# Kernel optimization log

Measured on AMD Instinct MI355X. Metric: run time of the kernel, lower is better.

## Reference

```python
import jax, jax.numpy as jnp
import numpy as np

N, E, IN, H, L = 100000, 1600000, 128, 64, 3


def setup_inputs() -> dict:
    key = jax.random.key(0)
    ks = jax.random.split(key, 4)
    x = jax.random.normal(ks[0], (N, IN), dtype=jnp.float32)
    edge_index = jax.random.randint(ks[1], (2, E), 0, N, dtype=jnp.int32)
    enc_w = jax.random.normal(ks[2], (IN, H), dtype=jnp.float32) * 0.05
    enc_b = jnp.zeros((H,), jnp.float32)
    conv_w = jax.random.normal(ks[3], (L, H, H), dtype=jnp.float32) * 0.05
    conv_b = jnp.zeros((L, H), jnp.float32)
    return {"x": x, "edge_index": edge_index, "enc_w": enc_w, "enc_b": enc_b,
            "conv_w": conv_w, "conv_b": conv_b}


def _nuc(m):
    # nuclear norm of [N, C] via eigvals of the small C x C Gram matrix
    g = m.T @ m
    ev = jnp.linalg.eigvalsh(g)
    return jnp.sum(jnp.sqrt(jnp.clip(ev, 0.0, None)))


def _rank_diff(x):
    xn = x / _nuc(x)
    i = jnp.argmax(jnp.sum(jnp.abs(xn), axis=1))
    j = jnp.argmax(jnp.sum(jnp.abs(xn), axis=0))
    m0 = jnp.take(xn, i, axis=0)[None, :]   # [1, C]
    m1 = jnp.take(xn, j, axis=1)[:, None]   # [N, 1]
    m0 = jnp.where(jnp.take(m0[0], j) < 0.0, -m0, m0)
    xh = m1 @ m0
    xh = xh / _nuc(xh)
    return _nuc(xn - xh)


def _dirichlet(x, src, dst, deg, rw):
    # edges (src, dst) already include self loops; deg = degree(src)
    xn = x / jnp.linalg.norm(x)
    if rw:
        d = xn[src] - xn[dst]
        e = jnp.sum(d * d)
    else:
        xs = xn * jax.lax.rsqrt(deg)[:, None]
        d = xs[src] - xs[dst]
        coef = jax.lax.rsqrt(deg[src] * deg[dst])
        e = jnp.sum(coef * jnp.sum(d * d, axis=1))
    return 0.5 * e


def reference(x, edge_index, enc_w, enc_b, conv_w, conv_b):
    n = x.shape[0]
    loops = jnp.arange(n, dtype=edge_index.dtype)
    src = jnp.concatenate([edge_index[0], loops])
    dst = jnp.concatenate([edge_index[1], loops])
    ones = jnp.ones(src.shape[0], x.dtype)
    deg_dst = jax.ops.segment_sum(ones, dst, num_segments=n)   # GCN norm degree
    dis = jax.lax.rsqrt(deg_dst)
    norm = dis[src] * dis[dst]
    deg_src = jax.ops.segment_sum(ones, src, num_segments=n)   # dirichlet degree

    h = x @ enc_w + enc_b                                      # encoder
    energies = [_dirichlet(jax.lax.stop_gradient(h), src, dst, deg_src, rw=False)]
    energies_sym = []
    ranks = []
    for i in range(L):
        # GCNConv: linear -> gather -> sym-normalized scatter-add -> bias
        xw = h @ conv_w[i]
        msg = xw[src] * norm[:, None]
        h = jax.ops.segment_sum(msg, dst, num_segments=n) + conv_b[i]
        h = jax.nn.relu(h)
        hs = jax.lax.stop_gradient(h)
        energies.append(_dirichlet(hs, src, dst, deg_src, rw=True))
        energies_sym.append(_dirichlet(hs, src, dst, deg_src, rw=False))
        ranks.append(_rank_diff(hs))
    return h, jnp.stack(energies), jnp.stack(energies_sym), jnp.stack(ranks)
```

## Files before the change

kernel.cpp:

```cpp
#include <hip/hip_runtime.h>

#define WF 64

__device__ inline float wredsum(float v) {
#pragma unroll
  for (int m = 32; m; m >>= 1) v += __shfl_xor(v, m, WF);
  return v;
}
__device__ inline float4 wredsum4(float4 v) {
#pragma unroll
  for (int m = 32; m; m >>= 1) {
    v.x += __shfl_xor(v.x, m, WF);
    v.y += __shfl_xor(v.y, m, WF);
    v.z += __shfl_xor(v.z, m, WF);
    v.w += __shfl_xor(v.w, m, WF);
  }
  return v;
}
__device__ inline float wredmin(float v) {
#pragma unroll
  for (int m = 32; m; m >>= 1) v = fminf(v, __shfl_xor(v, m, WF));
  return v;
}
__device__ inline float wredmax(float v) {
#pragma unroll
  for (int m = 32; m; m >>= 1) v = fmaxf(v, __shfl_xor(v, m, WF));
  return v;
}

__device__ inline float fastrcp(float x) {
  float r;
  asm("v_rcp_f32 %0, %1" : "=v"(r) : "v"(x));
  return r;
}

__device__ inline void atomAddF(float* p, float v) { unsafeAtomicAdd(p, v); }

__global__ __launch_bounds__(256) void k_init(int* degs, int* degd, float* G,
                                              float* colsum, float* scal, int n) {
  int i = blockIdx.x * 256 + threadIdx.x;
  if (i < n) { degs[i] = 1; degd[i] = 1; }
  if (i < 3 * 4096) G[i] = 0.f;
  if (i < 3 * 64) colsum[i] = 0.f;
  if (i < 64) scal[i] = 0.f;
}

__global__ __launch_bounds__(256) void k_deg(const int* src, const int* dst,
                                             int* degs, int* degd, int e) {
  int i = blockIdx.x * 256 + threadIdx.x;
  int stride = gridDim.x * 256;
  for (; i < e; i += stride) {
    atomicAdd(&degs[src[i]], 1);
    atomicAdd(&degd[dst[i]], 1);
  }
}

__global__ __launch_bounds__(256) void k_nodescal(const int* degs, const int* degd,
                                                  float4* cn4, float* degsum, int n) {
  int i = blockIdx.x * 256 + threadIdx.x;
  if (i < n) {
    float fs = (float)degs[i], fd = (float)degd[i];
    float rs_ = rsqrtf(fs);
    float4 v;
    v.x = rsqrtf(fd);
    v.y = 1.f / fs;
    v.z = rs_;
    v.w = rs_ * rs_ * rs_;
    cn4[i] = v;
    degsum[i] = fs + fd;
  }
}

__global__ __launch_bounds__(256) void k_scan1(const int* degd, int* start, int* bsum, int n) {
  __shared__ int sb[256];
  int t = threadIdx.x, i = blockIdx.x * 256 + t;
  int v = (i < n) ? degd[i] : 0;
  sb[t] = v;
  __syncthreads();
  for (int off = 1; off < 256; off <<= 1) {
    int add = (t >= off) ? sb[t - off] : 0;
    __syncthreads();
    sb[t] += add;
    __syncthreads();
  }
  if (i < n) start[i] = sb[t] - v;
  if (t == 255) bsum[blockIdx.x] = sb[255];
}

__global__ __launch_bounds__(512) void k_scan2(int* bsum, int nb) {
  __shared__ int sb[512];
  int t = threadIdx.x;
  int v = (t < nb) ? bsum[t] : 0;
  sb[t] = v;
  __syncthreads();
  for (int off = 1; off < 512; off <<= 1) {
    int add = (t >= off) ? sb[t - off] : 0;
    __syncthreads();
    sb[t] += add;
    __syncthreads();
  }
  if (t < nb) bsum[t] = sb[t] - v;
}

__global__ __launch_bounds__(256) void k_scan3(int* start, const int* bsum, int* cursor,
                                               int n, int total) {
  int i = blockIdx.x * 256 + threadIdx.x;
  if (i < n) {
    int v = start[i] + bsum[i >> 8];
    start[i] = v;
    cursor[i] = v;
  }
  if (i == 0) start[n] = total;
}

__global__ __launch_bounds__(256) void k_scatter(const int* src, const int* dst, int* cursor,
                                                 int* csr, int e, int n) {
  int i = blockIdx.x * 256 + threadIdx.x;
  int tot = e + n;
  if (i >= tot) return;
  int s, d;
  if (i < e) { s = src[i]; d = dst[i]; } else { s = i - e; d = i - e; }
  int pos = atomicAdd(&cursor[d], 1);
  csr[pos] = s;
}

__global__ __launch_bounds__(256) void k_enc(const float* __restrict__ x,
                                             const float* __restrict__ W,
                                             const float* __restrict__ b,
                                             const float4* __restrict__ cn4,
                                             float* __restrict__ X,
                                             float* __restrict__ nsq,
                                             float4* __restrict__ P, int n) {
  __shared__ float Wl[128 * 64];
  for (int idx = threadIdx.x; idx < 128 * 64; idx += 256) Wl[idx] = W[idx];
  __syncthreads();
  int w = threadIdx.x >> 6, c = threadIdx.x & 63;
  float bc = b[c];
  for (int node = blockIdx.x * 4 + w; node < n; node += gridDim.x * 4) {
    const float4* xr4 = (const float4*)(x + (size_t)node * 128);
    float acc = bc;
#pragma unroll
    for (int k4 = 0; k4 < 32; k4++) {
      float4 xv = xr4[k4];
      acc += xv.x * Wl[(k4 * 4 + 0) * 64 + c];
      acc += xv.y * Wl[(k4 * 4 + 1) * 64 + c];
      acc += xv.z * Wl[(k4 * 4 + 2) * 64 + c];
      acc += xv.w * Wl[(k4 * 4 + 3) * 64 + c];
    }
    X[(size_t)node * 64 + c] = acc;
    float r = wredsum(acc * acc);
    if (c == 0) {
      nsq[node] = r;
      float4 c4 = cn4[node];
      P[node] = make_float4(c4.x, c4.y, c4.z, r * c4.w);
    }
  }
}

template <int AGGC>
__device__ inline void gather4(const float* __restrict__ H, const float4* __restrict__ P,
                               const int* __restrict__ csr, int k0, int k1, int g, int l16,
                               float4& agg0, float4& agg1, float4& aggC,
                               float& su, float& sv) {
  int kk = k0 + g;
  int last = k1 - 1;
  int s0 = csr[min(kk, last)];
  int s1 = csr[min(kk + 4, last)];
  int s2 = csr[min(kk + 8, last)];
  int s3 = csr[min(kk + 12, last)];
  while (kk < k1) {
    int kn = kk + 16;
    float4 h0 = *(const float4*)(H + (size_t)s0 * 64 + 4 * l16);
    float4 h1 = *(const float4*)(H + (size_t)s1 * 64 + 4 * l16);
    float4 h2 = *(const float4*)(H + (size_t)s2 * 64 + 4 * l16);
    float4 h3 = *(const float4*)(H + (size_t)s3 * 64 + 4 * l16);
    float4 Q0 = P[s0], Q1 = P[s1], Q2 = P[s2], Q3 = P[s3];
    s0 = csr[min(kn, last)];
    s1 = csr[min(kn + 4, last)];
    s2 = csr[min(kn + 8, last)];
    s3 = csr[min(kn + 12, last)];
    float m1 = (kk + 4 < k1) ? 1.f : 0.f;
    float m2 = (kk + 8 < k1) ? 1.f : 0.f;
    float m3 = (kk + 12 < k1) ? 1.f : 0.f;
    agg0.x += h0.x; agg0.y += h0.y; agg0.z += h0.z; agg0.w += h0.w;
    agg1.x = fmaf(h0.x, Q0.y, agg1.x); agg1.y = fmaf(h0.y, Q0.y, agg1.y);
    agg1.z = fmaf(h0.z, Q0.y, agg1.z); agg1.w = fmaf(h0.w, Q0.y, agg1.w);
    if (AGGC) {
      aggC.x = fmaf(h0.x, Q0.x, aggC.x); aggC.y = fmaf(h0.y, Q0.x, aggC.y);
      aggC.z = fmaf(h0.z, Q0.x, aggC.z); aggC.w = fmaf(h0.w, Q0.x, aggC.w);
    }
    su += Q0.w; sv += Q0.z;
    {
      float y = Q1.y * m1;
      agg0.x = fmaf(h1.x, m1, agg0.x); agg0.y = fmaf(h1.y, m1, agg0.y);
      agg0.z = fmaf(h1.z, m1, agg0.z); agg0.w = fmaf(h1.w, m1, agg0.w);
      agg1.x = fmaf(h1.x, y, agg1.x); agg1.y = fmaf(h1.y, y, agg1.y);
      agg1.z = fmaf(h1.z, y, agg1.z); agg1.w = fmaf(h1.w, y, agg1.w);
      if (AGGC) {
        float xq = Q1.x * m1;
        aggC.x = fmaf(h1.x, xq, aggC.x); aggC.y = fmaf(h1.y, xq, aggC.y);
        aggC.z = fmaf(h1.z, xq, aggC.z); aggC.w = fmaf(h1.w, xq, aggC.w);
      }
      su = fmaf(Q1.w, m1, su); sv = fmaf(Q1.z, m1, sv);
    }
    {
      float y = Q2.y * m2;
      agg0.x = fmaf(h2.x, m2, agg0.x); agg0.y = fmaf(h2.y, m2, agg0.y);
      agg0.z = fmaf(h2.z, m2, agg0.z); agg0.w = fmaf(h2.w, m2, agg0.w);
      agg1.x = fmaf(h2.x, y, agg1.x); agg1.y = fmaf(h2.y, y, agg1.y);
      agg1.z = fmaf(h2.z, y, agg1.z); agg1.w = fmaf(h2.w, y, agg1.w);
      if (AGGC) {
        float xq = Q2.x * m2;
        aggC.x = fmaf(h2.x, xq, aggC.x); aggC.y = fmaf(h2.y, xq, aggC.y);
        aggC.z = fmaf(h2.z, xq, aggC.z); aggC.w = fmaf(h2.w, xq, aggC.w);
      }
      su = fmaf(Q2.w, m2, su); sv = fmaf(Q2.z, m2, sv);
    }
    {
      float y = Q3.y * m3;
      agg0.x = fmaf(h3.x, m3, agg0.x); agg0.y = fmaf(h3.y, m3, agg0.y);
      agg0.z = fmaf(h3.z, m3, agg0.z); agg0.w = fmaf(h3.w, m3, agg0.w);
      agg1.x = fmaf(h3.x, y, agg1.x); agg1.y = fmaf(h3.y, y, agg1.y);
      agg1.z = fmaf(h3.z, y, agg1.z); agg1.w = fmaf(h3.w, y, agg1.w);
      if (AGGC) {
        float xq = Q3.x * m3;
        aggC.x = fmaf(h3.x, xq, aggC.x); aggC.y = fmaf(h3.y, xq, aggC.y);
        aggC.z = fmaf(h3.z, xq, aggC.z); aggC.w = fmaf(h3.w, xq, aggC.w);
      }
      su = fmaf(Q3.w, m3, su); sv = fmaf(Q3.z, m3, sv);
    }
    kk = kn;
  }
}

__global__ __launch_bounds__(256) void k_convpass(
    const float* __restrict__ H, const float4* __restrict__ P,
    const float* __restrict__ nsq, const float* __restrict__ degsum,
    const float4* __restrict__ cn4, const int* __restrict__ start,
    const int* __restrict__ csr, const float* __restrict__ W,
    const float* __restrict__ bias, float* __restrict__ T,
    float4* __restrict__ Pn, float* __restrict__ nsqN,
    float* __restrict__ scal5, float* __restrict__ G, float* __restrict__ colsum,
    float* __restrict__ bmv, int* __restrict__ bmi, int n) {
  __shared__ float Wl[4096];
  __shared__ float rowbuf[4][64];
  __shared__ float red[4][5];
  __shared__ float colred[4][64];
  __shared__ float mvs[4];
  __shared__ int mis[4];
  int t = threadIdx.x, w = t >> 6, lane = t & 63, g = lane >> 4, l16 = lane & 15;
  for (int i = t; i < 4096; i += 256) Wl[i] = W[i];
  __syncthreads();
  float a0 = 0.f, a1 = 0.f, a2 = 0.f, a3 = 0.f, a4 = 0.f;
  float Greg[16];
#pragma unroll
  for (int k = 0; k < 16; k++) Greg[k] = 0.f;
  float cacc = 0.f, best = -1.f;
  int bi = 0;
  float bc = bias[lane];
  int wid = blockIdx.x * 4 + w, nw = gridDim.x * 4;
  int iters = (n + nw - 1) / nw;
  for (int it = 0; it < iters; it++) {
    int d = wid + it * nw;
    bool valid = d < n;
    float tv = 0.f;
    if (valid) {
      int k0 = start[d], k1 = start[d + 1];
      float4 hd = *(const float4*)(H + (size_t)d * 64 + 4 * l16);
      float4 pd = P[d];
      float nqd = nsq[d];
      float dsum = degsum[d];
      float4 agg0 = {0.f, 0.f, 0.f, 0.f};
      float4 agg1 = {0.f, 0.f, 0.f, 0.f};
      float4 aggC = {0.f, 0.f, 0.f, 0.f};
      float su = 0.f, sv = 0.f;
      gather4<1>(H, P, csr, k0, k1, g, l16, agg0, agg1, aggC, su, sv);
      float td0 = agg0.x * hd.x + agg0.y * hd.y + agg0.z * hd.z + agg0.w * hd.w;
      float td1 = agg1.x * hd.x + agg1.y * hd.y + agg1.z * hd.z + agg1.w * hd.w;
      float4 r4 = wredsum4(make_float4(td0, td1, su, sv));
      float dot1 = r4.x, dot2 = r4.y;
      su = r4.z * 0.0625f;
      sv = r4.w * 0.0625f;
      a0 += dsum * nqd;
      a1 += dot1;
      a2 += pd.z * su + pd.w * sv;
      a3 += pd.y * dot2;
      a4 += nqd;
      aggC.x += __shfl_xor(aggC.x, 16); aggC.y += __shfl_xor(aggC.y, 16);
      aggC.z += __shfl_xor(aggC.z, 16); aggC.w += __shfl_xor(aggC.w, 16);
      aggC.x += __shfl_xor(aggC.x, 32); aggC.y += __shfl_xor(aggC.y, 32);
      aggC.z += __shfl_xor(aggC.z, 32); aggC.w += __shfl_xor(aggC.w, 32);
      float mv = 0.f;
#pragma unroll
      for (int kq = 0; kq < 16; kq++) {
        float ax = __shfl(aggC.x, kq, 16);
        float ay = __shfl(aggC.y, kq, 16);
        float az = __shfl(aggC.z, kq, 16);
        float aw = __shfl(aggC.w, kq, 16);
        mv += ax * Wl[(4 * kq + 0) * 64 + lane];
        mv += ay * Wl[(4 * kq + 1) * 64 + lane];
        mv += az * Wl[(4 * kq + 2) * 64 + lane];
        mv += aw * Wl[(4 * kq + 3) * 64 + lane];
      }
      tv = fmaxf(fmaf(pd.x, mv, bc), 0.f);
      T[(size_t)d * 64 + lane] = tv;
      float r = wredsum(tv * tv);
      float atv = fabsf(tv);
      cacc += atv;
      float rsum = wredsum(atv);
      if (rsum > best) { best = rsum; bi = d; }
      if (lane == 0) {
        nsqN[d] = r;
        float4 c4 = cn4[d];
        Pn[d] = make_float4(c4.x, c4.y, c4.z, r * c4.w);
      }
    }
    rowbuf[w][lane] = tv;
    __syncthreads();
#pragma unroll
    for (int rr = 0; rr < 4; rr++) {
      float hj = rowbuf[rr][lane];
#pragma unroll
      for (int k = 0; k < 16; k++) Greg[k] = fmaf(rowbuf[rr][w + 4 * k], hj, Greg[k]);
    }
    __syncthreads();
  }
#pragma unroll
  for (int k = 0; k < 16; k++) atomAddF(&G[(w + 4 * k) * 64 + lane], Greg[k]);
  colred[w][lane] = cacc;
  if (lane == 0) {
    red[w][0] = a0; red[w][1] = a1; red[w][2] = a2; red[w][3] = a3; red[w][4] = a4;
    mvs[w] = best; mis[w] = bi;
  }
  __syncthreads();
  if (t < 64) {
    float cs = colred[0][t] + colred[1][t] + colred[2][t] + colred[3][t];
    atomAddF(&colsum[t], cs);
  }
  if (t == 0) {
#pragma unroll
    for (int j = 0; j < 5; j++)
      atomAddF(&scal5[j], red[0][j] + red[1][j] + red[2][j] + red[3][j]);
    float bv = mvs[0]; int bix = mis[0];
    for (int q = 1; q < 4; q++)
      if (mvs[q] > bv || (mvs[q] == bv && mis[q] < bix)) { bv = mvs[q]; bix = mis[q]; }
    bmv[blockIdx.x] = bv;
    bmi[blockIdx.x] = bix;
  }
}

__global__ __launch_bounds__(64) void k_finalize(const float* T, const float* bmv,
                                                 const int* bmi, int nblocks,
                                                 const float* colsum, float* rowslot,
                                                 int* jstar, int n) {
  int t = threadIdx.x;
  float bv = -1.f;
  int bix = 0x7fffffff;
  for (int b = t; b < nblocks; b += 64) {
    float v = bmv[b]; int ix = bmi[b];
    if (v > bv || (v == bv && ix < bix)) { bv = v; bix = ix; }
  }
#pragma unroll
  for (int m = 32; m; m >>= 1) {
    float ov = __shfl_xor(bv, m); int oi = __shfl_xor(bix, m);
    if (ov > bv || (ov == bv && oi < bix)) { bv = ov; bix = oi; }
  }
  float cv = colsum[t];
  int cj = t;
#pragma unroll
  for (int m = 32; m; m >>= 1) {
    float ov = __shfl_xor(cv, m); int oj = __shfl_xor(cj, m);
    if (ov > cv || (ov == cv && oj < cj)) { cv = ov; cj = oj; }
  }
  if (t == 0) jstar[0] = cj;
  rowslot[t] = T[(size_t)bix * 64 + t];
}

__device__ float tridiag_sumsqrt(float (*A)[65], float* vbuf, float* wbuf,
                                 float (*wpart)[64], float2* de, float* esh, int t) {
  bool w0 = (t < 64);
  int lane = t & 63, w4 = t >> 6;
  for (int k = 0; k < 62; k++) {
    float beta = 0.f;
    if (w0) {
      float acol = A[t][k];
      float xs = (t >= k + 2) ? acol : 0.f;
      float sigma = wredsum(xs * xs);
      float x1 = __shfl(acol, k + 1, WF);
      float alpha = -copysignf(sqrtf(fmaf(x1, x1, sigma)), x1);
      float v1 = x1 - alpha;
      float vv = fmaf(v1, v1, sigma);
      beta = (vv > 1e-37f) ? 2.f / vv : 0.f;
      vbuf[t] = (t == k + 1) ? v1 : xs;
      if (t == 0) esh[k] = alpha;
    }
    __syncthreads();
    {
      float s0 = 0.f, s1 = 0.f, s2 = 0.f, s3 = 0.f;
#pragma unroll
      for (int i2 = 0; i2 < 4; i2++) {
        int j = w4 + 16 * i2;
        s0 = fmaf(A[lane][j], vbuf[j], s0);
        s1 = fmaf(A[lane][j + 4], vbuf[j + 4], s1);
        s2 = fmaf(A[lane][j + 8], vbuf[j + 8], s2);
        s3 = fmaf(A[lane][j + 12], vbuf[j + 12], s3);
      }
      wpart[w4][lane] = (s0 + s1) + (s2 + s3);
    }
    __syncthreads();
    if (w0) {
      float p = beta * (wpart[0][t] + wpart[1][t] + wpart[2][t] + wpart[3][t]);
      float dot = wredsum(vbuf[t] * p);
      float K = 0.5f * beta * dot;
      wbuf[t] = fmaf(-K, vbuf[t], p);
    }
    __syncthreads();
    {
      float vj = vbuf[lane], wj = wbuf[lane];
#pragma unroll
      for (int i2 = 0; i2 < 16; i2++) {
        int i = w4 + 4 * i2;
        A[i][lane] -= vbuf[i] * wj + wbuf[i] * vj;
      }
    }
    __syncthreads();
  }
  if (t == 0) { esh[62] = A[63][62]; esh[63] = 0.f; }
  __syncthreads();
  float gmin = 0.f, gmax = 0.f;
  if (w0) {
    float dt = A[t][t];
    float ep = (t >= 1) ? esh[t - 1] : 0.f;
    float en = (t <= 62) ? esh[t] : 0.f;
    de[t] = make_float2(dt, ep * ep);
    float rad = fabsf(ep) + fabsf(en);
    gmin = wredmin(dt - rad);
    gmax = wredmax(dt + rad);
  }
  __syncthreads();
  float lam = 0.f;
  if (w0) {
    float range = gmax - gmin;
    float lo = gmin - 1e-3f * range - 1e-30f;
    float hi = gmax + 1e-3f * range + 1e-30f;
    for (int it = 0; it < 30; it++) {
      float mid = 0.5f * (lo + hi);
      float q = de[0].x - mid;
      int cnt = (q < 0.f) ? 1 : 0;
      for (int i = 1; i < 64; i++) {
        float2 dc = de[i];
        float qq = (dc.x - mid) - dc.y * fastrcp(q);
        q = (fabsf(qq) < 1e-30f) ? -1e-30f : qq;
        cnt += (q < 0.f) ? 1 : 0;
      }
      if (cnt > t) hi = mid; else lo = mid;
    }
    lam = 0.5f * (lo + hi);
  }
  float svv = w0 ? sqrtf(fmaxf(lam, 0.f)) : 0.f;
  return wredsum(svv);
}

__global__ __launch_bounds__(256, 4) void k_final(
    const float* __restrict__ H, const float4* __restrict__ P,
    const float* __restrict__ nsq, const float* __restrict__ degsum,
    const int* __restrict__ start, const int* __restrict__ csr,
    float* __restrict__ scal5, const float* __restrict__ Gbase,
    const float* __restrict__ rowslot, const int* __restrict__ jstar,
    float* __restrict__ rankOut, int n, int nbE) {
  __shared__ float A[64][65];
  __shared__ float vbuf[64], wbuf[64], esh[64];
  __shared__ float wpart[4][64];
  __shared__ float2 de[64];
  __shared__ float u[64], m0[64];
  __shared__ float shn;
  __shared__ float red[4][5];
  int t = threadIdx.x, w = t >> 6, lane = t & 63, g = lane >> 4, l16 = lane & 15;
  if (blockIdx.x < 3) {
    int l = blockIdx.x;
    const float* Gl = Gbase + l * 4096;
    for (int idx = t; idx < 4096; idx += 256) A[idx >> 6][idx & 63] = Gl[idx];
    __syncthreads();
    float nuc1 = tridiag_sumsqrt(A, vbuf, wbuf, wpart, de, esh, t);
    if (t == 0) shn = nuc1;
    __syncthreads();
    float s = 1.f / shn;
    int js = jstar[l];
    if (t < 64) {
      float rv = rowslot[l * 64 + t];
      float rn2 = wredsum(rv * rv);
      float sign = (rowslot[l * 64 + js] < 0.f) ? -1.f : 1.f;
      m0[t] = sign * rv * rsqrtf(rn2);
      u[t] = s * Gl[t * 64 + js] * rsqrtf(Gl[js * 64 + js]);
    }
    __syncthreads();
    float s2 = s * s;
    for (int idx = t; idx < 4096; idx += 256) {
      int i = idx >> 6, j = idx & 63;
      A[i][j] = s2 * Gl[idx] - u[i] * m0[j] - m0[i] * u[j] + m0[i] * m0[j];
    }
    __syncthreads();
    float nuc2 = tridiag_sumsqrt(A, vbuf, wbuf, wpart, de, esh, t);
    if (t == 0) rankOut[l] = nuc2;
    return;
  }
  float a0 = 0.f, a1 = 0.f, a2 = 0.f, a3 = 0.f, a4 = 0.f;
  int wid = (blockIdx.x - 3) * 4 + w, nw = nbE * 4;
  for (int d = wid; d < n; d += nw) {
    int k0 = start[d], k1 = start[d + 1];
    float4 hd = *(const float4*)(H + (size_t)d * 64 + 4 * l16);
    float4 pd = P[d];
    float nqd = nsq[d];
    float dsum = degsum[d];
    float4 agg0 = {0.f, 0.f, 0.f, 0.f};
    float4 agg1 = {0.f, 0.f, 0.f, 0.f};
    float4 aggC = {0.f, 0.f, 0.f, 0.f};
    float su = 0.f, sv = 0.f;
    gather4<0>(H, P, csr, k0, k1, g, l16, agg0, agg1, aggC, su, sv);
    float td0 = agg0.x * hd.x + agg0.y * hd.y + agg0.z * hd.z + agg0.w * hd.w;
    float td1 = agg1.x * hd.x + agg1.y * hd.y + agg1.z * hd.z + agg1.w * hd.w;
    float4 r4 = wredsum4(make_float4(td0, td1, su, sv));
    a0 += dsum * nqd;
    a1 += r4.x;
    a2 += pd.z * (r4.z * 0.0625f) + pd.w * (r4.w * 0.0625f);
    a3 += pd.y * r4.y;
    a4 += nqd;
  }
  if (lane == 0) {
    red[w][0] = a0; red[w][1] = a1; red[w][2] = a2; red[w][3] = a3; red[w][4] = a4;
  }
  __syncthreads();
  if (t == 0) {
#pragma unroll
    for (int j = 0; j < 5; j++)
      atomAddF(&scal5[j], red[0][j] + red[1][j] + red[2][j] + red[3][j]);
  }
}

__global__ __launch_bounds__(64) void k_epi(const float* scal, float* outsc) {
  if (threadIdx.x == 0) {
    for (int st = 0; st < 4; st++) {
      const float* a = scal + 5 * st;
      float inv = 1.f / a[4];
      float rw = 0.5f * (a[0] - 2.f * a[1]) * inv;
      float sym = 0.5f * (a[2] - 2.f * a[3]) * inv;
      if (st == 0) outsc[0] = sym;
      else { outsc[st] = rw; outsc[3 + st] = sym; }
    }
    for (int l = 0; l < 3; l++) outsc[7 + l] = scal[20 + l];
  }
}

extern "C" void kernel_launch(void* const* d_in, const int* in_sizes, int n_in,
                              void* d_out, int out_size, void* d_ws, size_t ws_size,
                              hipStream_t stream) {
  const float* x      = (const float*)d_in[0];
  const int*   ei     = (const int*)d_in[1];
  const float* enc_w  = (const float*)d_in[2];
  const float* enc_b  = (const float*)d_in[3];
  const float* conv_w = (const float*)d_in[4];
  const float* conv_b = (const float*)d_in[5];
  const int n = in_sizes[0] / 128;
  const int e = in_sizes[1] / 2;
  const int* src = ei;
  const int* dst = ei + e;
  float* OUT = (float*)d_out;
  float* outsc = OUT + (size_t)n * 64;

  char* p = (char*)d_ws;
  auto alloc = [&](size_t bytes) -> char* {
    char* r = p;
    p += (bytes + 255) & ~size_t(255);
    return r;
  };
  float*  X      = (float*)alloc((size_t)n * 64 * 4);
  float*  Yf     = (float*)alloc((size_t)n * 64 * 4);
  int*    csr    = (int*)alloc((size_t)(e + n) * 4);
  int*    degs   = (int*)alloc((size_t)n * 4);
  int*    degd   = (int*)alloc((size_t)n * 4);
  float4* cn4    = (float4*)alloc((size_t)n * 16);
  float*  degsum = (float*)alloc((size_t)n * 4);
  int*    start  = (int*)alloc((size_t)(n + 1) * 4);
  int*    cursor = (int*)alloc((size_t)n * 4);
  int*    bsum   = (int*)alloc(4096);
  float*  nsqA   = (float*)alloc((size_t)n * 4);
  float*  nsqB   = (float*)alloc((size_t)n * 4);
  float4* Pa     = (float4*)alloc((size_t)n * 16);
  float4* Pb     = (float4*)alloc((size_t)n * 16);
  float*  G      = (float*)alloc(3 * 4096 * 4);
  float*  colsum = (float*)alloc(3 * 64 * 4);
  float*  bmv    = (float*)alloc(2048 * 4);
  int*    bmi    = (int*)alloc(2048 * 4);
  float*  rowslot= (float*)alloc(3 * 64 * 4);
  float*  scal   = (float*)alloc(64 * 4);
  int*    ij     = (int*)alloc(64 * 4);

  int nb = (n + 255) / 256;
  const int NBL = 2048;

  k_init<<<nb, 256, 0, stream>>>(degs, degd, G, colsum, scal, n);
  k_deg<<<2048, 256, 0, stream>>>(src, dst, degs, degd, e);
  k_nodescal<<<nb, 256, 0, stream>>>(degs, degd, cn4, degsum, n);
  k_scan1<<<nb, 256, 0, stream>>>(degd, start, bsum, n);
  k_scan2<<<1, 512, 0, stream>>>(bsum, nb);
  k_scan3<<<nb, 256, 0, stream>>>(start, bsum, cursor, n, e + n);
  k_scatter<<<(e + n + 255) / 256, 256, 0, stream>>>(src, dst, cursor, csr, e, n);
  k_enc<<<NBL, 256, 0, stream>>>(x, enc_w, enc_b, cn4, X, nsqA, Pa, n);

  k_convpass<<<NBL, 256, 0, stream>>>(X, Pa, nsqA, degsum, cn4, start, csr,
                                      conv_w, conv_b, Yf, Pb, nsqB,
                                      scal, G, colsum, bmv, bmi, n);
  k_finalize<<<1, 64, 0, stream>>>(Yf, bmv, bmi, NBL, colsum, rowslot, ij, n);

  k_convpass<<<NBL, 256, 0, stream>>>(Yf, Pb, nsqB, degsum, cn4, start, csr,
                                      conv_w + 4096, conv_b + 64, X, Pa, nsqA,
                                      scal + 5, G + 4096, colsum + 64, bmv, bmi, n);
  k_finalize<<<1, 64, 0, stream>>>(X, bmv, bmi, NBL, colsum + 64, rowslot + 64, ij + 1, n);

  k_convpass<<<NBL, 256, 0, stream>>>(X, Pa, nsqA, degsum, cn4, start, csr,
                                      conv_w + 2 * 4096, conv_b + 128, OUT, Pb, nsqB,
                                      scal + 10, G + 2 * 4096, colsum + 128, bmv, bmi, n);
  k_finalize<<<1, 64, 0, stream>>>(OUT, bmv, bmi, NBL, colsum + 128, rowslot + 128, ij + 2, n);

  k_final<<<NBL + 3, 256, 0, stream>>>(OUT, Pb, nsqB, degsum, start, csr,
                                       scal + 15, G, rowslot, ij, scal + 20, n, NBL);
  k_epi<<<1, 64, 0, stream>>>(scal, outsc);
}
```

Baseline: 1.435 ms.

## Overlap per-layer rank eigen-solve with next conv pass via extra block

Each layer's rank computation (two Householder tridiagonalizations and bisection eigenvalue solves) now runs in one extra block appended to the following conv pass, instead of three blocks serialized at the end in k_final. This hides the long single-block eigen-solve latency behind the bulk graph gather work. The Householder update also skips already-reduced rows and columns to cut redundant shared-memory work. Shared memory is unioned between the conv and rank layouts, and the grid-stride in convpass now uses nbC rather than gridDim.

```diff
diff --git a/kernel.cpp b/kernel.cpp
--- a/kernel.cpp
+++ b/kernel.cpp
@@ -35,6 +35,27 @@
 }
 
 __device__ inline void atomAddF(float* p, float v) { unsafeAtomicAdd(p, v); }
+
+struct ConvS {
+  float Wl[4096];
+  float rowbuf[4][64];
+  float red[4][5];
+  float colred[4][64];
+  float mvs[4];
+  int mis[4];
+};
+struct RankS {
+  float A[64][65];
+  float vbuf[64], wbuf[64], esh[64];
+  float wpart[4][64];
+  float2 de[64];
+  float u[64], m0[64];
+  float shn;
+};
+union SmemU {
+  ConvS c;
+  RankS r;
+};
 
 __global__ __launch_bounds__(256) void k_init(int* degs, int* degd, float* G,
                                               float* colsum, float* scal, int n) {
@@ -233,6 +254,119 @@
   }
 }
 
+__device__ float tridiag_sumsqrt(RankS& S, int t) {
+  bool w0 = (t < 64);
+  int lane = t & 63, w4 = t >> 6;
+  for (int k = 0; k < 62; k++) {
+    float beta = 0.f;
+    if (w0) {
+      float acol = S.A[t][k];
+      float xs = (t >= k + 2) ? acol : 0.f;
+      float sigma = wredsum(xs * xs);
+      float x1 = __shfl(acol, k + 1, WF);
+      float alpha = -copysignf(sqrtf(fmaf(x1, x1, sigma)), x1);
+      float v1 = x1 - alpha;
+      float vv = fmaf(v1, v1, sigma);
+      beta = (vv > 1e-37f) ? 2.f / vv : 0.f;
+      S.vbuf[t] = (t == k + 1) ? v1 : xs;
+      if (t == 0) S.esh[k] = alpha;
+    }
+    __syncthreads();
+    {
+      float s0 = 0.f, s1 = 0.f, s2 = 0.f, s3 = 0.f;
+#pragma unroll
+      for (int i2 = 0; i2 < 4; i2++) {
+        int j = w4 + 16 * i2;
+        if (j > k)      s0 = fmaf(S.A[lane][j], S.vbuf[j], s0);
+        if (j + 4 > k)  s1 = fmaf(S.A[lane][j + 4], S.vbuf[j + 4], s1);
+        if (j + 8 > k)  s2 = fmaf(S.A[lane][j + 8], S.vbuf[j + 8], s2);
+        if (j + 12 > k) s3 = fmaf(S.A[lane][j + 12], S.vbuf[j + 12], s3);
+      }
+      S.wpart[w4][lane] = (s0 + s1) + (s2 + s3);
+    }
+    __syncthreads();
+    if (w0) {
+      float p = beta * (S.wpart[0][t] + S.wpart[1][t] + S.wpart[2][t] + S.wpart[3][t]);
+      float dot = wredsum(S.vbuf[t] * p);
+      float K = 0.5f * beta * dot;
+      S.wbuf[t] = fmaf(-K, S.vbuf[t], p);
+    }
+    __syncthreads();
+    {
+      float vj = S.vbuf[lane], wj = S.wbuf[lane];
+#pragma unroll
+      for (int i2 = 0; i2 < 16; i2++) {
+        int i = w4 + 4 * i2;
+        if (i > k) S.A[i][lane] -= S.vbuf[i] * wj + S.wbuf[i] * vj;
+      }
+    }
+    __syncthreads();
+  }
+  if (t == 0) { S.esh[62] = S.A[63][62]; S.esh[63] = 0.f; }
+  __syncthreads();
+  float gmin = 0.f, gmax = 0.f;
+  if (w0) {
+    float dt = S.A[t][t];
+    float ep = (t >= 1) ? S.esh[t - 1] : 0.f;
+    float en = (t <= 62) ? S.esh[t] : 0.f;
+    S.de[t] = make_float2(dt, ep * ep);
+    float rad = fabsf(ep) + fabsf(en);
+    gmin = wredmin(dt - rad);
+    gmax = wredmax(dt + rad);
+  }
+  __syncthreads();
+  float lam = 0.f;
+  if (w0) {
+    float range = gmax - gmin;
+    float lo = gmin - 1e-3f * range - 1e-30f;
+    float hi = gmax + 1e-3f * range + 1e-30f;
+    for (int it = 0; it < 30; it++) {
+      float mid = 0.5f * (lo + hi);
+      float q = S.de[0].x - mid;
+      int cnt = (q < 0.f) ? 1 : 0;
+      for (int i = 1; i < 64; i++) {
+        float2 dc = S.de[i];
+        float qq = (dc.x - mid) - dc.y * fastrcp(q);
+        q = (fabsf(qq) < 1e-30f) ? -1e-30f : qq;
+        cnt += (q < 0.f) ? 1 : 0;
+      }
+      if (cnt > t) hi = mid; else lo = mid;
+    }
+    lam = 0.5f * (lo + hi);
+  }
+  float svv = w0 ? sqrtf(fmaxf(lam, 0.f)) : 0.f;
+  return wredsum(svv);
+}
+
+__device__ void rank_block(RankS& S, const float* __restrict__ Gl,
+                           const float* __restrict__ rowslot_l,
+                           const int* __restrict__ jstar_l,
+                           float* __restrict__ rankOut_l, int t) {
+  for (int idx = t; idx < 4096; idx += 256) S.A[idx >> 6][idx & 63] = Gl[idx];
+  __syncthreads();
+  float nuc1 = tridiag_sumsqrt(S, t);
+  if (t == 0) S.shn = nuc1;
+  __syncthreads();
+  float s = 1.f / S.shn;
+  int js = jstar_l[0];
+  if (t < 64) {
+    float rv = rowslot_l[t];
+    float rn2 = wredsum(rv * rv);
+    float sign = (rowslot_l[js] < 0.f) ? -1.f : 1.f;
+    S.m0[t] = sign * rv * rsqrtf(rn2);
+    S.u[t] = s * Gl[t * 64 + js] * rsqrtf(Gl[js * 64 + js]);
+  }
+  __syncthreads();
+  float s2 = s * s;
+  for (int idx = t; idx < 4096; idx += 256) {
+    int i = idx >> 6, j = idx & 63;
+    S.A[i][j] = s2 * Gl[idx] - S.u[i] * S.m0[j] - S.m0[i] * S.u[j] + S.m0[i] * S.m0[j];
+  }
+  __syncthreads();
+  float nuc2 = tridiag_sumsqrt(S, t);
+  if (t == 0) rankOut_l[0] = nuc2;
+}
+
 __global__ __launch_bounds__(256) void k_convpass(
     const float* __restrict__ H, const float4* __restrict__ P,
     const float* __restrict__ nsq, const float* __restrict__ degsum,
@@ -241,15 +375,16 @@
     const float* __restrict__ bias, float* __restrict__ T,
     float4* __restrict__ Pn, float* __restrict__ nsqN,
     float* __restrict__ scal5, float* __restrict__ G, float* __restrict__ colsum,
-    float* __restrict__ bmv, int* __restrict__ bmi, int n) {
-  __shared__ float Wl[4096];
-  __shared__ float rowbuf[4][64];
-  __shared__ float red[4][5];
-  __shared__ float colred[4][64];
-  __shared__ float mvs[4];
-  __shared__ int mis[4];
+    float* __restrict__ bmv, int* __restrict__ bmi, int n, int nbC,
+    const float* __restrict__ Gr, const float* __restrict__ rowslotR,
+    const int* __restrict__ jstarR, float* __restrict__ rankOutR) {
+  __shared__ SmemU sm;
   int t = threadIdx.x, w = t >> 6, lane = t & 63, g = lane >> 4, l16 = lane & 15;
-  for (int i = t; i < 4096; i += 256) Wl[i] = W[i];
+  if ((int)blockIdx.x >= nbC) {
+    rank_block(sm.r, Gr, rowslotR, jstarR, rankOutR, t);
+    return;
+  }
+  for (int i = t; i < 4096; i += 256) sm.c.Wl[i] = W[i];
   __syncthreads();
   float a0 = 0.f, a1 = 0.f, a2 = 0.f, a3 = 0.f, a4 = 0.f;
   float Greg[16];
@@ -258,7 +393,7 @@
   float cacc = 0.f, best = -1.f;
   int bi = 0;
   float bc = bias[lane];
-  int wid = blockIdx.x * 4 + w, nw = gridDim.x * 4;
+  int wid = blockIdx.x * 4 + w, nw = nbC * 4;
   int iters = (n + nw - 1) / nw;
   for (int it = 0; it < iters; it++) {
     int d = wid + it * nw;
@@ -297,10 +432,10 @@
         float ay = __shfl(aggC.y, kq, 16);
         float az = __shfl(aggC.z, kq, 16);
         float aw = __shfl(aggC.w, kq, 16);
-        mv += ax * Wl[(4 * kq + 0) * 64 + lane];
-        mv += ay * Wl[(4 * kq + 1) * 64 + lane];
-        mv += az * Wl[(4 * kq + 2) * 64 + lane];
-        mv += aw * Wl[(4 * kq + 3) * 64 + lane];
+        mv += ax * sm.c.Wl[(4 * kq + 0) * 64 + lane];
+        mv += ay * sm.c.Wl[(4 * kq + 1) * 64 + lane];
+        mv += az * sm.c.Wl[(4 * kq + 2) * 64 + lane];
+        mv += aw * sm.c.Wl[(4 * kq + 3) * 64 + lane];
       }
       tv = fmaxf(fmaf(pd.x, mv, bc), 0.f);
       T[(size_t)d * 64 + lane] = tv;
@@ -315,35 +450,38 @@
         Pn[d] = make_float4(c4.x, c4.y, c4.z, r * c4.w);
       }
     }
-    rowbuf[w][lane] = tv;
+    sm.c.rowbuf[w][lane] = tv;
     __syncthreads();
 #pragma unroll
     for (int rr = 0; rr < 4; rr++) {
-      float hj = rowbuf[rr][lane];
-#pragma unroll
-      for (int k = 0; k < 16; k++) Greg[k] = fmaf(rowbuf[rr][w + 4 * k], hj, Greg[k]);
+      float hj = sm.c.rowbuf[rr][lane];
+#pragma unroll
+      for (int k = 0; k < 16; k++) Greg[k] = fmaf(sm.c.rowbuf[rr][w + 4 * k], hj, Greg[k]);
     }
     __syncthreads();
   }
 #pragma unroll
   for (int k = 0; k < 16; k++) atomAddF(&G[(w + 4 * k) * 64 + lane], Greg[k]);
-  colred[w][lane] = cacc;
+  sm.c.colred[w][lane] = cacc;
   if (lane == 0) {
-    red[w][0] = a0; red[w][1] = a1; red[w][2] = a2; red[w][3] = a3; red[w][4] = a4;
-    mvs[w] = best; mis[w] = bi;
+    sm.c.red[w][0] = a0; sm.c.red[w][1] = a1; sm.c.red[w][2] = a2;
+    sm.c.red[w][3] = a3; sm.c.red[w][4] = a4;
+    sm.c.mvs[w] = best; sm.c.mis[w] = bi;
   }
   __syncthreads();
   if (t < 64) {
-    float cs = colred[0][t] + colred[1][t] + colred[2][t] + colred[3][t];
+    float cs = sm.c.colred[0][t] + sm.c.colred[1][t] + sm.c.colred[2][t] + sm.c.colred[3][t];
     atomAddF(&colsum[t], cs);
   }
   if (t == 0) {
 #pragma unroll
     for (int j = 0; j < 5; j++)
-      atomAddF(&scal5[j], red[0][j] + red[1][j] + red[2][j] + red[3][j]);
-    float bv = mvs[0]; int bix = mis[0];
+      atomAddF(&scal5[j], sm.c.red[0][j] + sm.c.red[1][j] + sm.c.red[2][j] + sm.c.red[3][j]);
+    float bv = sm.c.mvs[0]; int bix = sm.c.mis[0];
     for (int q = 1; q < 4; q++)
-      if (mvs[q] > bv || (mvs[q] == bv && mis[q] < bix)) { bv = mvs[q]; bix = mis[q]; }
+      if (sm.c.mvs[q] > bv || (sm.c.mvs[q] == bv && sm.c.mis[q] < bix)) {
+        bv = sm.c.mvs[q]; bix = sm.c.mis[q];
+      }
     bmv[blockIdx.x] = bv;
     bmi[blockIdx.x] = bix;
   }
@@ -376,136 +514,21 @@
   rowslot[t] = T[(size_t)bix * 64 + t];
 }
 
-__device__ float tridiag_sumsqrt(float (*A)[65], float* vbuf, float* wbuf,
-                                 float (*wpart)[64], float2* de, float* esh, int t) {
-  bool w0 = (t < 64);
-  int lane = t & 63, w4 = t >> 6;
-  for (int k = 0; k < 62; k++) {
-    float beta = 0.f;
-    if (w0) {
-      float acol = A[t][k];
-      float xs = (t >= k + 2) ? acol : 0.f;
-      float sigma = wredsum(xs * xs);
-      float x1 = __shfl(acol, k + 1, WF);
-      float alpha = -copysignf(sqrtf(fmaf(x1, x1, sigma)), x1);
-      float v1 = x1 - alpha;
-      float vv = fmaf(v1, v1, sigma);
-      beta = (vv > 1e-37f) ? 2.f / vv : 0.f;
-      vbuf[t] = (t == k + 1) ? v1 : xs;
-      if (t == 0) esh[k] = alpha;
-    }
-    __syncthreads();
-    {
-      float s0 = 0.f, s1 = 0.f, s2 = 0.f, s3 = 0.f;
-#pragma unroll
-      for (int i2 = 0; i2 < 4; i2++) {
-        int j = w4 + 16 * i2;
-        s0 = fmaf(A[lane][j], vbuf[j], s0);
-        s1 = fmaf(A[lane][j + 4], vbuf[j + 4], s1);
-        s2 = fmaf(A[lane][j + 8], vbuf[j + 8], s2);
-        s3 = fmaf(A[lane][j + 12], vbuf[j + 12], s3);
-      }
-      wpart[w4][lane] = (s0 + s1) + (s2 + s3);
-    }
-    __syncthreads();
-    if (w0) {
-      float p = beta * (wpart[0][t] + wpart[1][t] + wpart[2][t] + wpart[3][t]);
-      float dot = wredsum(vbuf[t] * p);
-      float K = 0.5f * beta * dot;
-      wbuf[t] = fmaf(-K, vbuf[t], p);
-    }
-    __syncthreads();
-    {
-      float vj = vbuf[lane], wj = wbuf[lane];
-#pragma unroll
-      for (int i2 = 0; i2 < 16; i2++) {
-        int i = w4 + 4 * i2;
-        A[i][lane] -= vbuf[i] * wj + wbuf[i] * vj;
-      }
-    }
-    __syncthreads();
-  }
-  if (t == 0) { esh[62] = A[63][62]; esh[63] = 0.f; }
-  __syncthreads();
-  float gmin = 0.f, gmax = 0.f;
-  if (w0) {
-    float dt = A[t][t];
-    float ep = (t >= 1) ? esh[t - 1] : 0.f;
-    float en = (t <= 62) ? esh[t] : 0.f;
-    de[t] = make_float2(dt, ep * ep);
-    float rad = fabsf(ep) + fabsf(en);
-    gmin = wredmin(dt - rad);
-    gmax = wredmax(dt + rad);
-  }
-  __syncthreads();
-  float lam = 0.f;
-  if (w0) {
-    float range = gmax - gmin;
-    float lo = gmin - 1e-3f * range - 1e-30f;
-    float hi = gmax + 1e-3f * range + 1e-30f;
-    for (int it = 0; it < 30; it++) {
-      float mid = 0.5f * (lo + hi);
-      float q = de[0].x - mid;
-      int cnt = (q < 0.f) ? 1 : 0;
-      for (int i = 1; i < 64; i++) {
-        float2 dc = de[i];
-        float qq = (dc.x - mid) - dc.y * fastrcp(q);
-        q = (fabsf(qq) < 1e-30f) ? -1e-30f : qq;
-        cnt += (q < 0.f) ? 1 : 0;
-      }
-      if (cnt > t) hi = mid; else lo = mid;
-    }
-    lam = 0.5f * (lo + hi);
-  }
-  float svv = w0 ? sqrtf(fmaxf(lam, 0.f)) : 0.f;
-  return wredsum(svv);
-}
-
-__global__ __launch_bounds__(256, 4) void k_final(
+__global__ __launch_bounds__(256) void k_final(
     const float* __restrict__ H, const float4* __restrict__ P,
     const float* __restrict__ nsq, const float* __restrict__ degsum,
     const int* __restrict__ start, const int* __restrict__ csr,
-    float* __restrict__ scal5, const float* __restrict__ Gbase,
-    const float* __restrict__ rowslot, const int* __restrict__ jstar,
-    float* __restrict__ rankOut, int n, int nbE) {
-  __shared__ float A[64][65];
-  __shared__ float vbuf[64], wbuf[64], esh[64];
-  __shared__ float wpart[4][64];
-  __shared__ float2 de[64];
-  __shared__ float u[64], m0[64];
-  __shared__ float shn;
-  __shared__ float red[4][5];
+    float* __restrict__ scal5, const float* __restrict__ Gr,
+    const float* __restrict__ rowslotR, const int* __restrict__ jstarR,
+    float* __restrict__ rankOutR, int n, int nbE) {
+  __shared__ SmemU sm;
   int t = threadIdx.x, w = t >> 6, lane = t & 63, g = lane >> 4, l16 = lane & 15;
-  if (blockIdx.x < 3) {
-    int l = blockIdx.x;
-    const float* Gl = Gbase + l * 4096;
-    for (int idx = t; idx < 4096; idx += 256) A[idx >> 6][idx & 63] = Gl[idx];
-    __syncthreads();
-    float nuc1 = tridiag_sumsqrt(A, vbuf, wbuf, wpart, de, esh, t);
-    if (t == 0) shn = nuc1;
-    __syncthreads();
-    float s = 1.f / shn;
-    int js = jstar[l];
-    if (t < 64) {
-      float rv = rowslot[l * 64 + t];
-      float rn2 = wredsum(rv * rv);
-      float sign = (rowslot[l * 64 + js] < 0.f) ? -1.f : 1.f;
-      m0[t] = sign * rv * rsqrtf(rn2);
-      u[t] = s * Gl[t * 64 + js] * rsqrtf(Gl[js * 64 + js]);
-    }
-    __syncthreads();
-    float s2 = s * s;
-    for (int idx = t; idx < 4096; idx += 256) {
-      int i = idx >> 6, j = idx & 63;
-      A[i][j] = s2 * Gl[idx] - u[i] * m0[j] - m0[i] * u[j] + m0[i] * m0[j];
-    }
-    __syncthreads();
-    float nuc2 = tridiag_sumsqrt(A, vbuf, wbuf, wpart, de, esh, t);
-    if (t == 0) rankOut[l] = nuc2;
+  if (blockIdx.x == 0) {
+    rank_block(sm.r, Gr, rowslotR, jstarR, rankOutR, t);
     return;
   }
   float a0 = 0.f, a1 = 0.f, a2 = 0.f, a3 = 0.f, a4 = 0.f;
-  int wid = (blockIdx.x - 3) * 4 + w, nw = nbE * 4;
+  int wid = (blockIdx.x - 1) * 4 + w, nw = nbE * 4;
   for (int d = wid; d < n; d += nw) {
     int k0 = start[d], k1 = start[d + 1];
     float4 hd = *(const float4*)(H + (size_t)d * 64 + 4 * l16);
@@ -527,13 +550,14 @@
     a4 += nqd;
   }
   if (lane == 0) {
-    red[w][0] = a0; red[w][1] = a1; red[w][2] = a2; red[w][3] = a3; red[w][4] = a4;
+    sm.c.red[w][0] = a0; sm.c.red[w][1] = a1; sm.c.red[w][2] = a2;
+    sm.c.red[w][3] = a3; sm.c.red[w][4] = a4;
   }
   __syncthreads();
   if (t == 0) {
 #pragma unroll
     for (int j = 0; j < 5; j++)
-      atomAddF(&scal5[j], red[0][j] + red[1][j] + red[2][j] + red[3][j]);
+      atomAddF(&scal5[j], sm.c.red[0][j] + sm.c.red[1][j] + sm.c.red[2][j] + sm.c.red[3][j]);
   }
 }
 
@@ -609,20 +633,24 @@
 
   k_convpass<<<NBL, 256, 0, stream>>>(X, Pa, nsqA, degsum, cn4, start, csr,
                                       conv_w, conv_b, Yf, Pb, nsqB,
-                                      scal, G, colsum, bmv, bmi, n);
+                                      scal, G, colsum, bmv, bmi, n, NBL,
+                                      nullptr, nullptr, nullptr, nullptr);
   k_finalize<<<1, 64, 0, stream>>>(Yf, bmv, bmi, NBL, colsum, rowslot, ij, n);
 
-  k_convpass<<<NBL, 256, 0, stream>>>(Yf, Pb, nsqB, degsum, cn4, start, csr,
-                                      conv_w + 4096, conv_b + 64, X, Pa, nsqA,
-                                      scal + 5, G + 4096, colsum + 64, bmv, bmi, n);
+  k_convpass<<<NBL + 1, 256, 0, stream>>>(Yf, Pb, nsqB, degsum, cn4, start, csr,
+                                          conv_w + 4096, conv_b + 64, X, Pa, nsqA,
+                                          scal + 5, G + 4096, colsum + 64, bmv, bmi, n, NBL,
+                                          G, rowslot, ij, scal + 20);
   k_finalize<<<1, 64, 0, stream>>>(X, bmv, bmi, NBL, colsum + 64, rowslot + 64, ij + 1, n);
 
-  k_convpass<<<NBL, 256, 0, stream>>>(X, Pa, nsqA, degsum, cn4, start, csr,
-                                      conv_w + 2 * 4096, conv_b + 128, OUT, Pb, nsqB,
-                                      scal + 10, G + 2 * 4096, colsum + 128, bmv, bmi, n);
+  k_convpass<<<NBL + 1, 256, 0, stream>>>(X, Pa, nsqA, degsum, cn4, start, csr,
+                                          conv_w + 2 * 4096, conv_b + 128, OUT, Pb, nsqB,
+                                          scal + 10, G + 2 * 4096, colsum + 128, bmv, bmi, n, NBL,
+                                          G + 4096, rowslot + 64, ij + 1, scal + 21);
   k_finalize<<<1, 64, 0, stream>>>(OUT, bmv, bmi, NBL, colsum + 128, rowslot + 128, ij + 2, n);
 
-  k_final<<<NBL + 3, 256, 0, stream>>>(OUT, Pb, nsqB, degsum, start, csr,
-                                       scal + 15, G, rowslot, ij, scal + 20, n, NBL);
+  k_final<<<NBL + 1, 256, 0, stream>>>(OUT, Pb, nsqB, degsum, start, csr,
+                                       scal + 15, G + 2 * 4096, rowslot + 128, ij + 2,
+                                       scal + 22, n, NBL);
   k_epi<<<1, 64, 0, stream>>>(scal, outsc);
 }
```

Result: slower. 2.054 ms (+43.2%).
